# Optimization experiments

Measured on AMD Instinct MI355X. Metric: run time of the kernel, lower is better.

The kernel has to match this reference:

```python
import jax, jax.numpy as jnp
import numpy as np

N = 10000   # nodes
E = 100000  # edges
B = 64      # graphs
HID = 128


def setup_inputs() -> dict:
    key = jax.random.key(0)
    ks = iter(jax.random.split(key, 64))
    def nrm(shape, s=0.1):
        return jax.random.normal(next(ks), shape, dtype=jnp.float32) * s
    inp = {}
    inp["x"] = nrm((N, 1), 1.0)
    inp["node_type"] = jax.random.randint(next(ks), (N,), 0, 2)
    inp["edge_index"] = jax.random.randint(next(ks), (2, E), 0, N)
    inp["edge_attr"] = nrm((E, 1), 1.0)
    inp["batch"] = jnp.sort(jax.random.randint(next(ks), (N,), 0, B))
    inp["vp_w"] = nrm((1, HID)); inp["vp_b"] = nrm((HID,))
    inp["type_emb"] = nrm((2, HID))
    def conv(pre, fin, h, c):
        inp[pre + "_wl"] = nrm((fin, h * c)); inp[pre + "_bl"] = nrm((h * c,))
        inp[pre + "_wr"] = nrm((fin, h * c)); inp[pre + "_br"] = nrm((h * c,))
        inp[pre + "_we"] = nrm((1, h * c));  inp[pre + "_att"] = nrm((h, c))
        inp[pre + "_bias"] = nrm((h * c if pre != "c3" else c,))
    conv("c1", HID, 8, HID)
    conv("c2", HID * 8, 2, HID)
    conv("c3", HID * 2, 1, HID)
    inp["m1_w"] = nrm((HID, HID)); inp["m1_b"] = nrm((HID,))
    inp["ln1_g"] = jnp.ones((HID,), jnp.float32); inp["ln1_b"] = jnp.zeros((HID,), jnp.float32)
    inp["m2_w"] = nrm((HID, HID // 2)); inp["m2_b"] = nrm((HID // 2,))
    inp["ln2_g"] = jnp.ones((HID // 2,), jnp.float32); inp["ln2_b"] = jnp.zeros((HID // 2,), jnp.float32)
    inp["m3_w"] = nrm((HID // 2, 1)); inp["m3_b"] = nrm((1,))
    return inp


def _gatv2(x, src, dst, ea, wl, bl, wr, br, we, att, bias, heads, out_ch, concat):
    """PyG GATv2Conv (eval mode): add self-loops (edge_attr fill='mean' over dst),
    attn = (att * leaky_relu(Wl x_src + Wr x_dst + We e)).sum(-1), segment-softmax
    over destination, scatter-add of alpha * Wl x_src."""
    n = x.shape[0]
    ones = jnp.ones((ea.shape[0], 1), ea.dtype)
    deg = jax.ops.segment_sum(ones, dst, num_segments=n)
    loop_attr = jax.ops.segment_sum(ea, dst, num_segments=n) / jnp.maximum(deg, 1.0)
    ar = jnp.arange(n, dtype=src.dtype)
    src2 = jnp.concatenate([src, ar])
    dst2 = jnp.concatenate([dst, ar])
    ea2 = jnp.concatenate([ea, loop_attr], axis=0)
    xl = (x @ wl + bl).reshape(n, heads, out_ch)   # source transform
    xr = (x @ wr + br).reshape(n, heads, out_ch)   # target transform
    e = (ea2 @ we).reshape(-1, heads, out_ch)      # [E2, H, C]
    msg = xl[src2]                                 # [E2, H, C]
    z = jax.nn.leaky_relu(msg + xr[dst2] + e, 0.2)
    score = jnp.einsum('ehc,hc->eh', z, att)       # [E2, H]
    smax = jax.ops.segment_max(score, dst2, num_segments=n)
    ex = jnp.exp(score - smax[dst2])
    denom = jax.ops.segment_sum(ex, dst2, num_segments=n)
    alpha = ex / denom[dst2]
    out = jax.ops.segment_sum(alpha[:, :, None] * msg, dst2, num_segments=n)
    out = out.reshape(n, heads * out_ch) if concat else out.mean(axis=1)
    return out + bias


def _layernorm(v, g, b):
    mu = v.mean(-1, keepdims=True)
    var = v.var(-1, keepdims=True)
    return (v - mu) / jnp.sqrt(var + 1e-5) * g + b


def reference(x, node_type, edge_index, edge_attr, batch,
              vp_w, vp_b, type_emb,
              c1_wl, c1_bl, c1_wr, c1_br, c1_we, c1_att, c1_bias,
              c2_wl, c2_bl, c2_wr, c2_br, c2_we, c2_att, c2_bias,
              c3_wl, c3_bl, c3_wr, c3_br, c3_we, c3_att, c3_bias,
              m1_w, m1_b, ln1_g, ln1_b, m2_w, m2_b, ln2_g, ln2_b, m3_w, m3_b):
    src, dst = edge_index[0], edge_index[1]
    h = x @ vp_w + vp_b + type_emb[node_type]
    h = jax.nn.leaky_relu(_gatv2(h, src, dst, edge_attr, c1_wl, c1_bl, c1_wr, c1_br, c1_we, c1_att, c1_bias, 8, HID, True), 0.2)
    h = jax.nn.leaky_relu(_gatv2(h, src, dst, edge_attr, c2_wl, c2_bl, c2_wr, c2_br, c2_we, c2_att, c2_bias, 2, HID, True), 0.2)
    h = jax.nn.leaky_relu(_gatv2(h, src, dst, edge_attr, c3_wl, c3_bl, c3_wr, c3_br, c3_we, c3_att, c3_bias, 1, HID, False), 0.2)
    # masked global mean pool over node_type == 0
    w = (node_type == 0).astype(h.dtype)
    sums = jax.ops.segment_sum(h * w[:, None], batch, num_segments=B)
    cnts = jax.ops.segment_sum(w, batch, num_segments=B)
    pooled = sums / jnp.maximum(cnts, 1.0)[:, None]
    h1 = jax.nn.leaky_relu(_layernorm(pooled @ m1_w + m1_b, ln1_g, ln1_b), 0.2)
    h2 = jax.nn.leaky_relu(_layernorm(h1 @ m2_w + m2_b, ln2_g, ln2_b), 0.2)
    return (h2 @ m3_w + m3_b).squeeze(-1)
```

## Files before the change

### kernel.cpp

```cpp
#include <hip/hip_runtime.h>
#include <math.h>

#define NN 10000
#define NE 100000
#define E2 (NE + NN)
#define NBATCH 64

typedef short bf16x8 __attribute__((ext_vector_type(8)));
typedef float f32x4 __attribute__((ext_vector_type(4)));

__device__ __forceinline__ float lrelu(float v){ return v > 0.f ? v : 0.2f*v; }

__device__ __forceinline__ unsigned short f2bf(float x){
  unsigned int u = __float_as_uint(x);
  u += 0x7fffu + ((u >> 16) & 1u);
  return (unsigned short)(u >> 16);
}
__device__ __forceinline__ float bf2f(unsigned short u){
  return __uint_as_float(((unsigned int)u) << 16);
}

__global__ __launch_bounds__(256) void prep_kernel(
    const float* __restrict__ vp_w, const float* __restrict__ vp_b,
    const float* __restrict__ type_emb,
    const float* __restrict__ c1_wl, const float* __restrict__ c1_bl,
    const float* __restrict__ c1_wr, const float* __restrict__ c1_br,
    float* __restrict__ Ul, float* __restrict__ CTl,
    float* __restrict__ Ur, float* __restrict__ CT2,
    const float* __restrict__ c2_wl, const float* __restrict__ c2_wr,
    const float* __restrict__ c3_wl, const float* __restrict__ c3_wr,
    unsigned short* __restrict__ W2lT, unsigned short* __restrict__ W2rT,
    unsigned short* __restrict__ W3lT, unsigned short* __restrict__ W3rT,
    float* __restrict__ zbase, int zero_words)
{
  __shared__ float t[64][65];
  int b = blockIdx.x;
  int tid = threadIdx.x;
  if (b < 144){
    const float* in; unsigned short* out; int K, N, idx;
    if (b < 64)      { in=c2_wl; out=W2lT; K=1024; N=256; idx=b; }
    else if (b <128) { in=c2_wr; out=W2rT; K=1024; N=256; idx=b-64; }
    else if (b <136) { in=c3_wl; out=W3lT; K=256;  N=128; idx=b-128; }
    else             { in=c3_wr; out=W3rT; K=256;  N=128; idx=b-136; }
    int K64 = K >> 6;
    int kx = idx % K64, nx = idx / K64;
    int k0 = kx*64, n0 = nx*64;
    int lr = tid >> 4;
    int lc = (tid & 15) * 4;
#pragma unroll
    for (int i=0;i<4;++i){
      int r = lr + i*16;
      float4 v = *(const float4*)(in + (size_t)(k0+r)*N + n0 + lc);
      t[r][lc+0]=v.x; t[r][lc+1]=v.y; t[r][lc+2]=v.z; t[r][lc+3]=v.w;
    }
    __syncthreads();
    int sr = tid >> 3;
    int sc = (tid & 7) * 8;
#pragma unroll
    for (int i=0;i<2;++i){
      int n = sr + i*32;
      unsigned short tmp[8];
#pragma unroll
      for (int j=0;j<8;++j) tmp[j] = f2bf(t[sc+j][n]);
      unsigned short* op = out + (size_t)(n0+n)*K + k0 + sc;
      *(ushort4*)op       = make_ushort4(tmp[0],tmp[1],tmp[2],tmp[3]);
      *(ushort4*)(op + 4) = make_ushort4(tmp[4],tmp[5],tmp[6],tmp[7]);
    }
  } else if (b < 148){
    int j = (b-144)*256 + tid;
    float ul=0.f, c0l=0.f, c1l=0.f, ur=0.f, c0r=0.f, c1r=0.f;
    for (int k=0; k<128; ++k){
      float a = c1_wl[k*1024 + j], bb = c1_wr[k*1024 + j];
      float vw = vp_w[k], vb = vp_b[k], t0 = type_emb[k], t1 = type_emb[128+k];
      ul += vw*a; ur += vw*bb;
      c0l += (vb+t0)*a; c1l += (vb+t1)*a;
      c0r += (vb+t0)*bb; c1r += (vb+t1)*bb;
    }
    float bl = c1_bl[j], br = c1_br[j];
    Ul[j]=ul; Ur[j]=ur;
    CTl[j]      = c0l + bl;
    CTl[1024+j] = c1l + bl;
    CT2[j]        = (c0l+bl) + (c0r+br);
    CT2[1024+j]   = (c0l+bl) + (c1r+br);
    CT2[2048+j]   = (c1l+bl) + (c0r+br);
    CT2[3072+j]   = (c1l+bl) + (c1r+br);
  } else {
    for (int i = (b-148)*256 + tid; i < zero_words; i += 32*256)
      zbase[i] = 0.f;
  }
}

__global__ void count_kernel(const int* __restrict__ dst, const float* __restrict__ ea,
                             int* __restrict__ deg, float* __restrict__ loop_sum){
  int e = blockIdx.x*256 + threadIdx.x;
  if (e < NE){
    int d = dst[e];
    atomicAdd(&deg[d], 1);
    atomicAdd(&loop_sum[d], ea[e]);
  }
}

__global__ __launch_bounds__(1024) void scan_kernel(const int* __restrict__ deg,
    const float* __restrict__ loop_sum, int* __restrict__ rowptr, float* __restrict__ loop_attr){
  __shared__ int wsum[16];
  __shared__ int carry_s;
  int tid = threadIdx.x;
  int lane = tid & 63, wid = tid >> 6;
  if (tid == 0) carry_s = 0;
  __syncthreads();
  for (int base = 0; base < NN; base += 1024){
    int i = base + tid;
    int v = (i < NN) ? deg[i] : 0;
    int incl = v;
#pragma unroll
    for (int off = 1; off < 64; off <<= 1){
      int t = __shfl_up(incl, off, 64);
      if (lane >= off) incl += t;
    }
    if (lane == 63) wsum[wid] = incl;
    __syncthreads();
    int pre = carry_s;
    for (int w = 0; w < wid; ++w) pre += wsum[w];
    if (i < NN){
      rowptr[i] = pre + incl - v;
      loop_attr[i] = loop_sum[i] / fmaxf((float)v, 1.f);
    }
    __syncthreads();
    if (tid == 0){
      int t = 0;
      for (int w = 0; w < 16; ++w) t += wsum[w];
      carry_s += t;
    }
    __syncthreads();
  }
  if (tid == 0) rowptr[NN] = carry_s;
}

__global__ void fill_kernel(const int* __restrict__ src, const int* __restrict__ dst,
                            const float* __restrict__ ea, const int* __restrict__ rowptr,
                            int* __restrict__ rowctr, int* __restrict__ srcs,
                            int* __restrict__ dsts, float* __restrict__ eav){
  int e = blockIdx.x*256 + threadIdx.x;
  if (e < NE){
    int d = dst[e];
    int p = rowptr[d] + atomicAdd(&rowctr[d], 1);
    srcs[p] = src[e];
    dsts[p] = d;
    eav[p] = ea[e];
  }
}

__global__ __launch_bounds__(256) void conv1_score(
    const int* __restrict__ srcs, const int* __restrict__ dsts, const float* __restrict__ eav,
    const float* __restrict__ loop_attr, const float* __restrict__ x, const int* __restrict__ ntype,
    const float* __restrict__ Ul, const float* __restrict__ Ur, const float* __restrict__ CT2,
    const float* __restrict__ we, const float* __restrict__ att,
    float* __restrict__ scores)
{
  __shared__ float ldsct[4096];
  int tid = threadIdx.x;
  for (int i = tid; i < 1024; i += 256)
    *(float4*)&ldsct[i*4] = *(const float4*)&CT2[i*4];
  int te = tid & 127;
  int sub = tid >> 7;
  int ch0 = te * 8;
  float ul[8], ur[8], wev[8], atv[8];
#pragma unroll
  for (int v=0; v<8; ++v){
    ul[v]=Ul[ch0+v]; ur[v]=Ur[ch0+v]; wev[v]=we[ch0+v]; atv[v]=att[ch0+v];
  }
  __syncthreads();
  for (int j = blockIdx.x*2 + sub; j < E2; j += gridDim.x*2){
    int s, d; float ea;
    if (j < NE){ s = srcs[j]; d = dsts[j]; ea = eav[j]; }
    else       { s = j - NE;  d = s;       ea = loop_attr[s]; }
    float xs = x[s], xn = x[d];
    int tt = ntype[s]*2 + ntype[d];
    const float* cp = &ldsct[tt*1024 + ch0];
    float4 c0 = *(const float4*)cp;
    float4 c1 = *(const float4*)(cp+4);
    float ct[8] = {c0.x,c0.y,c0.z,c0.w,c1.x,c1.y,c1.z,c1.w};
    float p = 0.f;
#pragma unroll
    for (int v=0; v<8; ++v){
      float z = fmaf(xs, ul[v], fmaf(xn, ur[v], fmaf(ea, wev[v], ct[v])));
      p += atv[v]*lrelu(z);
    }
#pragma unroll
    for (int mm=1; mm<16; mm<<=1) p += __shfl_xor(p, mm, 16);
    if ((te & 15) == 0) scores[(size_t)j*8 + (te>>4)] = p;
  }
}

__global__ __launch_bounds__(256) void conv1_agg(
    const int* __restrict__ rowptr, const int* __restrict__ srcs,
    const float* __restrict__ scores, const float* __restrict__ x, const int* __restrict__ ntype,
    const float* __restrict__ Ul, const float* __restrict__ CTl,
    const float* __restrict__ bias, unsigned short* __restrict__ out)
{
  int n = blockIdx.x;
  int tid = threadIdx.x;
  int h = tid >> 5, el = tid & 31;
  int beg = rowptr[n], deg = rowptr[n+1] - beg;
  int cnt = deg + 1;
  float m = -1e30f, l = 0.f, s1 = 0.f, s20 = 0.f;
  for (int i = el; i < cnt; i += 32){
    int pos; int s;
    if (i < deg){ pos = beg + i; s = srcs[pos]; }
    else        { pos = NE + n;  s = n; }
    float p = scores[(size_t)pos*8 + h];
    float xs = x[s];
    float w0 = (ntype[s] == 0) ? 1.f : 0.f;
    float mn = fmaxf(m, p), f = __expf(m-mn), pe = __expf(p-mn);
    l = l*f + pe; s1 = s1*f + pe*xs; s20 = s20*f + pe*w0; m = mn;
  }
#pragma unroll
  for (int off=1; off<32; off<<=1){
    float mb = __shfl_xor(m, off, 32), lb = __shfl_xor(l, off, 32);
    float s1b = __shfl_xor(s1, off, 32), s20b = __shfl_xor(s20, off, 32);
    float mn = fmaxf(m, mb), fa = __expf(m-mn), fb = __expf(mb-mn);
    l = l*fa + lb*fb; s1 = s1*fa + s1b*fb; s20 = s20*fa + s20b*fb; m = mn;
  }
  float inv = 1.f/l;
  s1 *= inv; s20 *= inv;
  float s21 = 1.f - s20;
  int ch0 = tid * 4;
  float4 u  = *(const float4*)(Ul + ch0);
  float4 t0 = *(const float4*)(CTl + ch0);
  float4 t1 = *(const float4*)(CTl + 1024 + ch0);
  float4 bi = *(const float4*)(bias + ch0);
  ushort4 o;
  o.x = f2bf(lrelu(s1*u.x + s20*t0.x + s21*t1.x + bi.x));
  o.y = f2bf(lrelu(s1*u.y + s20*t0.y + s21*t1.y + bi.y));
  o.z = f2bf(lrelu(s1*u.z + s20*t0.z + s21*t1.z + bi.z));
  o.w = f2bf(lrelu(s1*u.w + s20*t0.w + s21*t1.w + bi.w));
  *(ushort4*)(out + (size_t)n*1024 + ch0) = o;
}

template<int H, int THREADS, int VPT, bool ONLY0, bool OUTBF, bool INBF>
__global__ __launch_bounds__(THREADS) void conv_kernel(
    const int* __restrict__ rowptr, const int* __restrict__ srcs, const float* __restrict__ eav,
    const float* __restrict__ loop_attr, const int* __restrict__ ntype,
    const void* __restrict__ Xv, int stride, int xr_off,
    const float* __restrict__ we, const float* __restrict__ att, const float* __restrict__ bias,
    void* __restrict__ out)
{
  const int HC = THREADS*VPT;
  const int TPH = THREADS/H;
  int n = blockIdx.x;
  if (ONLY0 && ntype[n] != 0) return;
  int tid = threadIdx.x;
  int ch0 = tid * VPT;
  const float* Xf = (const float*)Xv;
  const unsigned short* Xb = (const unsigned short*)Xv;
  float wev[VPT], atv[VPT], biv[VPT], xrv[VPT];
#pragma unroll
  for (int v=0; v<VPT; ++v){
    int ch = ch0+v;
    wev[v]=we[ch]; atv[v]=att[ch]; biv[v]=bias[ch];
  }
  if constexpr (INBF){
    ushort4 q = *(const ushort4*)(Xb + (size_t)n*stride + xr_off + ch0);
    xrv[0]=bf2f(q.x); xrv[1]=bf2f(q.y); xrv[2]=bf2f(q.z); xrv[3]=bf2f(q.w);
  } else {
#pragma unroll
    for (int v=0; v<VPT; ++v) xrv[v]=Xf[(size_t)n*stride + xr_off + ch0+v];
  }
  float ms[4], ls[4], A[4][VPT];
#pragma unroll
  for (int k=0; k<4; ++k){
    ms[k] = -INFINITY; ls[k] = 0.f;
#pragma unroll
    for (int v=0; v<VPT; ++v) A[k][v] = 0.f;
  }
  int beg=rowptr[n], end=rowptr[n+1];
  float la = loop_attr[n];
  for (int j=beg; j<=end; j+=4){
    bool val[4]; int sx[4]; float ex[4];
#pragma unroll
    for (int k=0; k<4; ++k){
      int pos = j + k;
      val[k] = pos <= end;
      sx[k] = (!val[k] || pos == end) ? n : srcs[pos];
      ex[k] = !val[k] ? 0.f : (pos == end ? la : eav[pos]);
    }
    float xv[4][VPT];
#pragma unroll
    for (int k=0; k<4; ++k){
      if constexpr (INBF){
        ushort4 q = *(const ushort4*)(Xb + (size_t)sx[k]*stride + ch0);
        xv[k][0]=bf2f(q.x); xv[k][1]=bf2f(q.y); xv[k][2]=bf2f(q.z); xv[k][3]=bf2f(q.w);
      } else if constexpr (VPT == 4){
        float4 q = *(const float4*)(Xf + (size_t)sx[k]*stride + ch0);
        xv[k][0]=q.x; xv[k][1]=q.y; xv[k][2]=q.z; xv[k][3]=q.w;
      } else {
        float2 q = *(const float2*)(Xf + (size_t)sx[k]*stride + ch0);
        xv[k][0]=q.x; xv[k][1]=q.y;
      }
    }
    float p[4];
#pragma unroll
    for (int k=0; k<4; ++k){
      float acc = 0.f;
#pragma unroll
      for (int v=0; v<VPT; ++v)
        acc += atv[v]*lrelu(xv[k][v]+xrv[v]+ex[k]*wev[v]);
      p[k] = acc;
    }
#pragma unroll
    for (int mm=1; mm<TPH; mm<<=1){
#pragma unroll
      for (int k=0; k<4; ++k) p[k] += __shfl_xor(p[k], mm, 64);
    }
#pragma unroll
    for (int k=0; k<4; ++k){
      if (val[k]){
        float mn=fmaxf(ms[k],p[k]), sc=__expf(ms[k]-mn), pe=__expf(p[k]-mn);
        ls[k]=ls[k]*sc+pe; ms[k]=mn;
#pragma unroll
        for (int v=0; v<VPT; ++v) A[k][v]=A[k][v]*sc+pe*xv[k][v];
      }
    }
  }
#pragma unroll
  for (int k=1; k<4; ++k){
    float mn = fmaxf(ms[0], ms[k]);
    float fa = __expf(ms[0]-mn), fb = __expf(ms[k]-mn);
    ls[0] = ls[0]*fa + ls[k]*fb;
#pragma unroll
    for (int v=0; v<VPT; ++v) A[0][v] = A[0][v]*fa + A[k][v]*fb;
    ms[0] = mn;
  }
  float inv = 1.f/ls[0];
  size_t baseo=(size_t)n*HC+ch0;
  if constexpr (OUTBF){
    unsigned short* ob = (unsigned short*)out;
    ushort4 o;
    o.x = f2bf(lrelu(A[0][0]*inv+biv[0]));
    o.y = f2bf(lrelu(A[0][1]*inv+biv[1]));
    o.z = f2bf(lrelu(A[0][2]*inv+biv[2]));
    o.w = f2bf(lrelu(A[0][3]*inv+biv[3]));
    *(ushort4*)(ob + baseo) = o;
  } else {
    float* of = (float*)out;
#pragma unroll
    for (int v=0; v<VPT; ++v) of[baseo+v]=lrelu(A[0][v]*inv+biv[v]);
  }
}

template<bool OUTBF>
__global__ __launch_bounds__(256) void gemm_dual_lds(
    const short* __restrict__ Abf,
    const short* __restrict__ WlT, const short* __restrict__ WrT,
    const float* __restrict__ bl, const float* __restrict__ br,
    void* __restrict__ Out, int M, int K, int NcH, int cgrid, int rgrid)
{
  __shared__ short lds[12288];
  int id = blockIdx.x;
  int xcd = id & 7, slot = id >> 3;
  int nb = slot % cgrid;
  int rowgroup = (slot / cgrid) * 8 + xcd;
  if (rowgroup >= rgrid) return;
  int row0 = rowgroup * 128;
  int NC2 = 2*NcH;
  int halfx = NcH >> 6;
  int isR = nb >= halfx;
  const short* WT = isR ? WrT : WlT;
  const float* bias = isR ? br : bl;
  int col0 = (nb - (isR ? halfx : 0)) * 64;
  int gcol0 = nb * 64;
  int tid = threadIdx.x;
  int lane = tid & 63, wave = tid >> 6;
  int wm = wave >> 1, wn = wave & 1;
  int quad = lane >> 4, l16 = lane & 15;

  const short* asrc[4];
#pragma unroll
  for (int i=0;i<4;++i){
    int c = wave*256 + i*64 + lane;
    int m = c >> 3, j = c & 7;
    int gr = row0 + m; gr = gr < M ? gr : M-1;
    asrc[i] = Abf + (size_t)gr*K + ((j ^ (m & 7)) << 3);
  }
  const short* bsrc[2];
#pragma unroll
  for (int i=0;i<2;++i){
    int c = wave*128 + i*64 + lane;
    int nloc = c >> 3, j = c & 7;
    bsrc[i] = WT + (size_t)(col0 + nloc)*K + ((j ^ (nloc & 7)) << 3);
  }

  float biasv[2] = { bias[col0 + wn*32 + l16], bias[col0 + wn*32 + 16 + l16] };
  f32x4 acc[4][2];
#pragma unroll
  for (int f=0; f<4; ++f)
#pragma unroll
    for (int g=0; g<2; ++g) acc[f][g] = (f32x4){0.f,0.f,0.f,0.f};

  int niter = K >> 6;
  for (int it=0; it<niter; ++it){
    int k0 = it << 6;
#pragma unroll
    for (int i=0;i<4;++i)
      __builtin_amdgcn_global_load_lds(asrc[i] + k0, &lds[(wave*256 + i*64)*8], 16, 0, 0);
#pragma unroll
    for (int i=0;i<2;++i)
      __builtin_amdgcn_global_load_lds(bsrc[i] + k0, &lds[8192 + (wave*128 + i*64)*8], 16, 0, 0);
    __syncthreads();
#pragma unroll
    for (int s=0; s<2; ++s){
      int t = s*4 + quad;
      bf16x8 af[4], bfv[2];
#pragma unroll
      for (int f=0; f<4; ++f){
        int m = wm*64 + f*16 + l16;
        af[f] = *(const bf16x8*)&lds[m*64 + ((t ^ (m & 7)) << 3)];
      }
#pragma unroll
      for (int g=0; g<2; ++g){
        int nloc = wn*32 + g*16 + l16;
        bfv[g] = *(const bf16x8*)&lds[8192 + nloc*64 + ((t ^ (nloc & 7)) << 3)];
      }
#pragma unroll
      for (int f=0; f<4; ++f)
#pragma unroll
        for (int g=0; g<2; ++g)
          acc[f][g] = __builtin_amdgcn_mfma_f32_16x16x32_bf16(af[f], bfv[g], acc[f][g], 0,0,0);
    }
    __syncthreads();
  }

#pragma unroll
  for (int f=0; f<4; ++f){
    int rbase = row0 + wm*64 + f*16 + quad*4;
#pragma unroll
    for (int r=0; r<4; ++r){
      int rr = rbase + r;
      if (rr < M){
#pragma unroll
        for (int g=0; g<2; ++g){
          int cc = gcol0 + wn*32 + g*16 + l16;
          float val = acc[f][g][r] + biasv[g];
          if constexpr (OUTBF) ((unsigned short*)Out)[(size_t)rr*NC2 + cc] = f2bf(val);
          else                 ((float*)Out)[(size_t)rr*NC2 + cc] = val;
        }
      }
    }
  }
}

__device__ __forceinline__ int lbound(const int* __restrict__ a, int n, int key){
  int lo = 0, hi = n;
  while (lo < hi){ int mid = (lo+hi) >> 1; if (a[mid] < key) lo = mid+1; else hi = mid; }
  return lo;
}

__global__ __launch_bounds__(128) void head_kernel(
    const float* __restrict__ h3, const int* __restrict__ ntype, const int* __restrict__ batch,
    const float* __restrict__ m1w, const float* __restrict__ m1b,
    const float* __restrict__ g1, const float* __restrict__ b1,
    const float* __restrict__ m2w, const float* __restrict__ m2b,
    const float* __restrict__ g2, const float* __restrict__ b2,
    const float* __restrict__ m3w, const float* __restrict__ m3b,
    float* __restrict__ out)
{
  __shared__ float p[128];
  __shared__ float hb[128];
  __shared__ float red[128];
  int b = blockIdx.x, j = threadIdx.x;
  int lo = lbound(batch, NN, b);
  int hi = lbound(batch, NN, b+1);
  float s = 0.f, cnt = 0.f;
  int n = lo;
  for (; n + 3 < hi; n += 4){
    float w0 = (ntype[n]   == 0) ? 1.f : 0.f;
    float w1 = (ntype[n+1] == 0) ? 1.f : 0.f;
    float w2 = (ntype[n+2] == 0) ? 1.f : 0.f;
    float w3 = (ntype[n+3] == 0) ? 1.f : 0.f;
    s += w0*h3[(size_t)n*128 + j]     + w1*h3[(size_t)(n+1)*128 + j]
       + w2*h3[(size_t)(n+2)*128 + j] + w3*h3[(size_t)(n+3)*128 + j];
    cnt += w0 + w1 + w2 + w3;
  }
  for (; n < hi; ++n){
    float w = (ntype[n] == 0) ? 1.f : 0.f;
    s += w*h3[(size_t)n*128 + j];
    cnt += w;
  }
  p[j] = s / fmaxf(cnt, 1.f);
  __syncthreads();
  float a = m1b[j];
  for (int k=0; k<128; ++k) a += p[k]*m1w[k*128 + j];
  red[j] = a; __syncthreads();
  for (int off=64; off>0; off>>=1){ if (j<off) red[j] += red[j+off]; __syncthreads(); }
  float mu = red[0] * (1.f/128.f);
  __syncthreads();
  float d = a - mu;
  red[j] = d*d; __syncthreads();
  for (int off=64; off>0; off>>=1){ if (j<off) red[j] += red[j+off]; __syncthreads(); }
  float var = red[0] * (1.f/128.f);
  __syncthreads();
  hb[j] = lrelu(d * rsqrtf(var + 1e-5f) * g1[j] + b1[j]);
  __syncthreads();
  float a2 = 0.f;
  if (j < 64){
    a2 = m2b[j];
    for (int k=0; k<128; ++k) a2 += hb[k]*m2w[k*64 + j];
  }
  red[j] = (j<64) ? a2 : 0.f; __syncthreads();
  for (int off=64; off>0; off>>=1){ if (j<off) red[j] += red[j+off]; __syncthreads(); }
  float mu2 = red[0] * (1.f/64.f);
  __syncthreads();
  float d2 = a2 - mu2;
  red[j] = (j<64) ? d2*d2 : 0.f; __syncthreads();
  for (int off=64; off>0; off>>=1){ if (j<off) red[j] += red[j+off]; __syncthreads(); }
  float var2 = red[0] * (1.f/64.f);
  __syncthreads();
  if (j < 64) hb[j] = lrelu(d2 * rsqrtf(var2 + 1e-5f) * g2[j] + b2[j]);
  __syncthreads();
  if (j == 0){
    float o = m3b[0];
    for (int k=0; k<64; ++k) o += hb[k]*m3w[k];
    out[b] = o;
  }
}

extern "C" void kernel_launch(void* const* d_in, const int* in_sizes, int n_in,
                              void* d_out, int out_size, void* d_ws, size_t ws_size,
                              hipStream_t stream)
{
  const float* x        = (const float*)d_in[0];
  const int*   ntype    = (const int*)d_in[1];
  const int*   ei       = (const int*)d_in[2];
  const float* eattr    = (const float*)d_in[3];
  const int*   batch    = (const int*)d_in[4];
  const float* vp_w     = (const float*)d_in[5];
  const float* vp_b     = (const float*)d_in[6];
  const float* type_emb = (const float*)d_in[7];
  const float* c1_wl = (const float*)d_in[8];  const float* c1_bl = (const float*)d_in[9];
  const float* c1_wr = (const float*)d_in[10]; const float* c1_br = (const float*)d_in[11];
  const float* c1_we = (const float*)d_in[12]; const float* c1_att= (const float*)d_in[13];
  const float* c1_bias=(const float*)d_in[14];
  const float* c2_wl = (const float*)d_in[15]; const float* c2_bl = (const float*)d_in[16];
  const float* c2_wr = (const float*)d_in[17]; const float* c2_br = (const float*)d_in[18];
  const float* c2_we = (const float*)d_in[19]; const float* c2_att= (const float*)d_in[20];
  const float* c2_bias=(const float*)d_in[21];
  const float* c3_wl = (const float*)d_in[22]; const float* c3_bl = (const float*)d_in[23];
  const float* c3_wr = (const float*)d_in[24]; const float* c3_br = (const float*)d_in[25];
  const float* c3_we = (const float*)d_in[26]; const float* c3_att= (const float*)d_in[27];
  const float* c3_bias=(const float*)d_in[28];
  const float* m1_w = (const float*)d_in[29]; const float* m1_b = (const float*)d_in[30];
  const float* ln1_g= (const float*)d_in[31]; const float* ln1_b= (const float*)d_in[32];
  const float* m2_w = (const float*)d_in[33]; const float* m2_b = (const float*)d_in[34];
  const float* ln2_g= (const float*)d_in[35]; const float* ln2_b= (const float*)d_in[36];
  const float* m3_w = (const float*)d_in[37]; const float* m3_b = (const float*)d_in[38];
  const int* esrc = ei;
  const int* edst = ei + NE;
  float* outp = (float*)d_out;
  (void)in_sizes; (void)n_in; (void)out_size; (void)ws_size;

  char* w = (char*)d_ws;
  auto alloc = [&](size_t bytes) -> void* {
    void* p = (void*)w;
    w += (bytes + 255) & ~(size_t)255;
    return p;
  };
  unsigned short* h1bf = (unsigned short*)alloc((size_t)NN*1024*2);
  unsigned short* X2   = (unsigned short*)alloc((size_t)NN*512*2);
  unsigned short* h2bf = (unsigned short*)alloc((size_t)NN*256*2);
  float* X3   = (float*)alloc((size_t)NN*256*4);
  float* h3   = (float*)alloc((size_t)NN*128*4);
  unsigned short* W2lT = (unsigned short*)alloc((size_t)256*1024*2);
  unsigned short* W2rT = (unsigned short*)alloc((size_t)256*1024*2);
  unsigned short* W3lT = (unsigned short*)alloc((size_t)128*256*2);
  unsigned short* W3rT = (unsigned short*)alloc((size_t)128*256*2);
  float* Ul   = (float*)alloc(1024*4);
  float* CTl  = (float*)alloc(2048*4);
  float* Ur   = (float*)alloc(1024*4);
  float* CT2  = (float*)alloc(4096*4);
  float* scores = (float*)alloc((size_t)E2*8*4);
  const int zero_words = 3*NN;
  float* zbase = (float*)alloc((size_t)zero_words*4);
  int*   deg      = (int*)zbase;
  int*   rowctr   = (int*)(zbase + NN);
  float* loop_sum = zbase + 2*NN;
  float* loop_attr= (float*)alloc((size_t)NN*4);
  int*   rowptr   = (int*)alloc((size_t)(NN+1)*4);
  int*   srcs     = (int*)alloc((size_t)NE*4);
  int*   dsts     = (int*)alloc((size_t)NE*4);
  float* eav      = (float*)alloc((size_t)NE*4);

  prep_kernel<<<180, 256, 0, stream>>>(vp_w, vp_b, type_emb,
      c1_wl, c1_bl, c1_wr, c1_br, Ul, CTl, Ur, CT2,
      c2_wl, c2_wr, c3_wl, c3_wr, W2lT, W2rT, W3lT, W3rT,
      zbase, zero_words);
  count_kernel<<<(NE+255)/256, 256, 0, stream>>>(edst, eattr, deg, loop_sum);
  scan_kernel<<<1, 1024, 0, stream>>>(deg, loop_sum, rowptr, loop_attr);
  fill_kernel<<<(NE+255)/256, 256, 0, stream>>>(esrc, edst, eattr, rowptr, rowctr,
                                                srcs, dsts, eav);
  conv1_score<<<2048, 256, 0, stream>>>(srcs, dsts, eav, loop_attr, x, ntype,
      Ul, Ur, CT2, c1_we, c1_att, scores);
  conv1_agg<<<NN, 256, 0, stream>>>(rowptr, srcs, scores, x, ntype,
      Ul, CTl, c1_bias, h1bf);
  gemm_dual_lds<true><<<640, 256, 0, stream>>>(
      (const short*)h1bf, (const short*)W2lT, (const short*)W2rT, c2_bl, c2_br,
      (void*)X2, NN, 1024, 256, 8, 79);
  conv_kernel<2,64,4,false,true,true><<<NN, 64, 0, stream>>>(rowptr, srcs, eav, loop_attr, ntype,
      (const void*)X2, 512, 256, c2_we, c2_att, c2_bias, h2bf);
  gemm_dual_lds<false><<<320, 256, 0, stream>>>(
      (const short*)h2bf, (const short*)W3lT, (const short*)W3rT, c3_bl, c3_br,
      (void*)X3, NN, 256, 128, 4, 79);
  conv_kernel<1,64,2,true,false,false><<<NN, 64, 0, stream>>>(rowptr, srcs, eav, loop_attr, ntype,
      (const void*)X3, 256, 128, c3_we, c3_att, c3_bias, h3);
  head_kernel<<<NBATCH, 128, 0, stream>>>(h3, ntype, batch, m1_w, m1_b, ln1_g, ln1_b,
                                          m2_w, m2_b, ln2_g, ln2_b, m3_w, m3_b, outp);
}
```

Before: 321.2 us.

## Split conv2/conv3 into edge-parallel score and node-parallel aggregate kernels

Replaces the single per-node online-softmax conv kernel for layers 2 and 3 with two passes. An edge-parallel kernel computes attention logits into a scores buffer, then a per-node kernel stages scores and sources in LDS, does a two-pass softmax, and aggregates with 4-way unrolled gathers. This is meant to remove the serial per-edge online-softmax rescaling and the latency of one block walking a long edge list, at the cost of a scores round trip through memory and an extra launch per layer. Nodes with in-degree above 1023 are silently truncated by the 1024-entry LDS cap.

```diff
diff --git a/kernel.cpp b/kernel.cpp
--- a/kernel.cpp
+++ b/kernel.cpp
@@ -237,115 +237,177 @@
   *(ushort4*)(out + (size_t)n*1024 + ch0) = o;
 }
 
-template<int H, int THREADS, int VPT, bool ONLY0, bool OUTBF, bool INBF>
-__global__ __launch_bounds__(THREADS) void conv_kernel(
-    const int* __restrict__ rowptr, const int* __restrict__ srcs, const float* __restrict__ eav,
+__global__ __launch_bounds__(256) void conv2_score(
+    const int* __restrict__ srcs, const int* __restrict__ dsts, const float* __restrict__ eav,
+    const float* __restrict__ loop_attr, const unsigned short* __restrict__ X2,
+    const float* __restrict__ we, const float* __restrict__ att,
+    float* __restrict__ scores2)
+{
+  int tid = threadIdx.x;
+  int lane = tid & 63, wv = tid >> 6;
+  int half = lane >> 5;
+  int ch0 = (lane & 31)*4 + half*128;
+  float wev[4], atv[4];
+#pragma unroll
+  for (int v=0; v<4; ++v){ wev[v]=we[ch0+v]; atv[v]=att[ch0+v]; }
+  for (int j = blockIdx.x*4 + wv; j < E2; j += gridDim.x*4){
+    int s, d; float ea;
+    if (j < NE){ s = srcs[j]; d = dsts[j]; ea = eav[j]; }
+    else       { s = j - NE;  d = s;       ea = loop_attr[s]; }
+    ushort4 ql = *(const ushort4*)(X2 + (size_t)s*512 + ch0);
+    ushort4 qr = *(const ushort4*)(X2 + (size_t)d*512 + 256 + ch0);
+    float xl[4] = {bf2f(ql.x),bf2f(ql.y),bf2f(ql.z),bf2f(ql.w)};
+    float xr[4] = {bf2f(qr.x),bf2f(qr.y),bf2f(qr.z),bf2f(qr.w)};
+    float p = 0.f;
+#pragma unroll
+    for (int v=0; v<4; ++v) p += atv[v]*lrelu(xl[v]+xr[v]+ea*wev[v]);
+#pragma unroll
+    for (int mm=1; mm<32; mm<<=1) p += __shfl_xor(p, mm, 64);
+    if ((lane & 31) == 0) scores2[(size_t)j*2 + half] = p;
+  }
+}
+
+__global__ __launch_bounds__(64) void conv2_agg(
+    const int* __restrict__ rowptr, const int* __restrict__ srcs,
+    const float* __restrict__ scores2, const unsigned short* __restrict__ X2,
+    const float* __restrict__ bias, unsigned short* __restrict__ out)
+{
+  __shared__ float pe2[1024][2];
+  __shared__ int es[1024];
+  int n = blockIdx.x, tid = threadIdx.x;
+  int beg = rowptr[n], deg = rowptr[n+1] - beg;
+  int cnt = deg + 1; if (cnt > 1024) cnt = 1024;
+  float m0 = -1e30f, m1 = -1e30f;
+  for (int i = tid; i < cnt; i += 64){
+    int pos = (i < deg) ? beg + i : NE + n;
+    float2 sc = *(const float2*)(scores2 + (size_t)pos*2);
+    pe2[i][0] = sc.x; pe2[i][1] = sc.y;
+    es[i] = (i < deg) ? srcs[pos] : n;
+    m0 = fmaxf(m0, sc.x); m1 = fmaxf(m1, sc.y);
+  }
+#pragma unroll
+  for (int off=1; off<64; off<<=1){
+    m0 = fmaxf(m0, __shfl_xor(m0, off, 64));
+    m1 = fmaxf(m1, __shfl_xor(m1, off, 64));
+  }
+  __syncthreads();
+  float l0 = 0.f, l1 = 0.f;
+  for (int i = tid; i < cnt; i += 64){
+    float e0 = __expf(pe2[i][0]-m0), e1 = __expf(pe2[i][1]-m1);
+    pe2[i][0] = e0; pe2[i][1] = e1;
+    l0 += e0; l1 += e1;
+  }
+#pragma unroll
+  for (int off=1; off<64; off<<=1){
+    l0 += __shfl_xor(l0, off, 64);
+    l1 += __shfl_xor(l1, off, 64);
+  }
+  __syncthreads();
+  int ch0 = tid*4, h = tid >> 5;
+  float inv = 1.f/((h==0) ? l0 : l1);
+  float acc[4] = {0.f,0.f,0.f,0.f};
+  int e = 0;
+  for (; e + 3 < cnt; e += 4){
+    float a0=pe2[e][h], a1=pe2[e+1][h], a2=pe2[e+2][h], a3=pe2[e+3][h];
+    int s0=es[e], s1=es[e+1], s2=es[e+2], s3=es[e+3];
+    ushort4 q0 = *(const ushort4*)(X2 + (size_t)s0*512 + ch0);
+    ushort4 q1 = *(const ushort4*)(X2 + (size_t)s1*512 + ch0);
+    ushort4 q2 = *(const ushort4*)(X2 + (size_t)s2*512 + ch0);
+    ushort4 q3 = *(const ushort4*)(X2 + (size_t)s3*512 + ch0);
+    acc[0] += a0*bf2f(q0.x) + a1*bf2f(q1.x) + a2*bf2f(q2.x) + a3*bf2f(q3.x);
+    acc[1] += a0*bf2f(q0.y) + a1*bf2f(q1.y) + a2*bf2f(q2.y) + a3*bf2f(q3.y);
+    acc[2] += a0*bf2f(q0.z) + a1*bf2f(q1.z) + a2*bf2f(q2.z) + a3*bf2f(q3.z);
+    acc[3] += a0*bf2f(q0.w) + a1*bf2f(q1.w) + a2*bf2f(q2.w) + a3*bf2f(q3.w);
+  }
+  for (; e < cnt; ++e){
+    float a = pe2[e][h];
+    ushort4 q = *(const ushort4*)(X2 + (size_t)es[e]*512 + ch0);
+    acc[0]+=a*bf2f(q.x); acc[1]+=a*bf2f(q.y); acc[2]+=a*bf2f(q.z); acc[3]+=a*bf2f(q.w);
+  }
+  ushort4 o;
+  o.x = f2bf(lrelu(acc[0]*inv + bias[ch0+0]));
+  o.y = f2bf(lrelu(acc[1]*inv + bias[ch0+1]));
+  o.z = f2bf(lrelu(acc[2]*inv + bias[ch0+2]));
+  o.w = f2bf(lrelu(acc[3]*inv + bias[ch0+3]));
+  *(ushort4*)(out + (size_t)n*256 + ch0) = o;
+}
+
+__global__ __launch_bounds__(256) void conv3_score(
+    const int* __restrict__ srcs, const int* __restrict__ dsts, const float* __restrict__ eav,
     const float* __restrict__ loop_attr, const int* __restrict__ ntype,
-    const void* __restrict__ Xv, int stride, int xr_off,
-    const float* __restrict__ we, const float* __restrict__ att, const float* __restrict__ bias,
-    void* __restrict__ out)
-{
-  const int HC = THREADS*VPT;
-  const int TPH = THREADS/H;
-  int n = blockIdx.x;
-  if (ONLY0 && ntype[n] != 0) return;
+    const float* __restrict__ X3,
+    const float* __restrict__ we, const float* __restrict__ att,
+    float* __restrict__ scores3)
+{
   int tid = threadIdx.x;
-  int ch0 = tid * VPT;
-  const float* Xf = (const float*)Xv;
-  const unsigned short* Xb = (const unsigned short*)Xv;
-  float wev[VPT], atv[VPT], biv[VPT], xrv[VPT];
-#pragma unroll
-  for (int v=0; v<VPT; ++v){
-    int ch = ch0+v;
-    wev[v]=we[ch]; atv[v]=att[ch]; biv[v]=bias[ch];
-  }
-  if constexpr (INBF){
-    ushort4 q = *(const ushort4*)(Xb + (size_t)n*stride + xr_off + ch0);
-    xrv[0]=bf2f(q.x); xrv[1]=bf2f(q.y); xrv[2]=bf2f(q.z); xrv[3]=bf2f(q.w);
-  } else {
-#pragma unroll
-    for (int v=0; v<VPT; ++v) xrv[v]=Xf[(size_t)n*stride + xr_off + ch0+v];
-  }
-  float ms[4], ls[4], A[4][VPT];
-#pragma unroll
-  for (int k=0; k<4; ++k){
-    ms[k] = -INFINITY; ls[k] = 0.f;
-#pragma unroll
-    for (int v=0; v<VPT; ++v) A[k][v] = 0.f;
-  }
-  int beg=rowptr[n], end=rowptr[n+1];
-  float la = loop_attr[n];
-  for (int j=beg; j<=end; j+=4){
-    bool val[4]; int sx[4]; float ex[4];
-#pragma unroll
-    for (int k=0; k<4; ++k){
-      int pos = j + k;
-      val[k] = pos <= end;
-      sx[k] = (!val[k] || pos == end) ? n : srcs[pos];
-      ex[k] = !val[k] ? 0.f : (pos == end ? la : eav[pos]);
-    }
-    float xv[4][VPT];
-#pragma unroll
-    for (int k=0; k<4; ++k){
-      if constexpr (INBF){
-        ushort4 q = *(const ushort4*)(Xb + (size_t)sx[k]*stride + ch0);
-        xv[k][0]=bf2f(q.x); xv[k][1]=bf2f(q.y); xv[k][2]=bf2f(q.z); xv[k][3]=bf2f(q.w);
-      } else if constexpr (VPT == 4){
-        float4 q = *(const float4*)(Xf + (size_t)sx[k]*stride + ch0);
-        xv[k][0]=q.x; xv[k][1]=q.y; xv[k][2]=q.z; xv[k][3]=q.w;
-      } else {
-        float2 q = *(const float2*)(Xf + (size_t)sx[k]*stride + ch0);
-        xv[k][0]=q.x; xv[k][1]=q.y;
-      }
-    }
-    float p[4];
-#pragma unroll
-    for (int k=0; k<4; ++k){
-      float acc = 0.f;
-#pragma unroll
-      for (int v=0; v<VPT; ++v)
-        acc += atv[v]*lrelu(xv[k][v]+xrv[v]+ex[k]*wev[v]);
-      p[k] = acc;
-    }
-#pragma unroll
-    for (int mm=1; mm<TPH; mm<<=1){
-#pragma unroll
-      for (int k=0; k<4; ++k) p[k] += __shfl_xor(p[k], mm, 64);
-    }
-#pragma unroll
-    for (int k=0; k<4; ++k){
-      if (val[k]){
-        float mn=fmaxf(ms[k],p[k]), sc=__expf(ms[k]-mn), pe=__expf(p[k]-mn);
-        ls[k]=ls[k]*sc+pe; ms[k]=mn;
-#pragma unroll
-        for (int v=0; v<VPT; ++v) A[k][v]=A[k][v]*sc+pe*xv[k][v];
-      }
-    }
-  }
-#pragma unroll
-  for (int k=1; k<4; ++k){
-    float mn = fmaxf(ms[0], ms[k]);
-    float fa = __expf(ms[0]-mn), fb = __expf(ms[k]-mn);
-    ls[0] = ls[0]*fa + ls[k]*fb;
-#pragma unroll
-    for (int v=0; v<VPT; ++v) A[0][v] = A[0][v]*fa + A[k][v]*fb;
-    ms[0] = mn;
-  }
-  float inv = 1.f/ls[0];
-  size_t baseo=(size_t)n*HC+ch0;
-  if constexpr (OUTBF){
-    unsigned short* ob = (unsigned short*)out;
-    ushort4 o;
-    o.x = f2bf(lrelu(A[0][0]*inv+biv[0]));
-    o.y = f2bf(lrelu(A[0][1]*inv+biv[1]));
-    o.z = f2bf(lrelu(A[0][2]*inv+biv[2]));
-    o.w = f2bf(lrelu(A[0][3]*inv+biv[3]));
-    *(ushort4*)(ob + baseo) = o;
-  } else {
-    float* of = (float*)out;
-#pragma unroll
-    for (int v=0; v<VPT; ++v) of[baseo+v]=lrelu(A[0][v]*inv+biv[v]);
-  }
+  int lane = tid & 63, wv = tid >> 6;
+  int ch0 = lane*2;
+  float wev[2] = {we[ch0], we[ch0+1]};
+  float atv[2] = {att[ch0], att[ch0+1]};
+  for (int j = blockIdx.x*4 + wv; j < E2; j += gridDim.x*4){
+    int s, d; float ea;
+    if (j < NE){ s = srcs[j]; d = dsts[j]; ea = eav[j]; }
+    else       { s = j - NE;  d = s;       ea = loop_attr[s]; }
+    if (ntype[d] != 0) continue;
+    float2 ql = *(const float2*)(X3 + (size_t)s*256 + ch0);
+    float2 qr = *(const float2*)(X3 + (size_t)d*256 + 128 + ch0);
+    float p = atv[0]*lrelu(ql.x+qr.x+ea*wev[0]) + atv[1]*lrelu(ql.y+qr.y+ea*wev[1]);
+#pragma unroll
+    for (int mm=1; mm<64; mm<<=1) p += __shfl_xor(p, mm, 64);
+    if (lane == 0) scores3[j] = p;
+  }
+}
+
+__global__ __launch_bounds__(64) void conv3_agg(
+    const int* __restrict__ rowptr, const int* __restrict__ srcs, const int* __restrict__ ntype,
+    const float* __restrict__ scores3, const float* __restrict__ X3,
+    const float* __restrict__ bias, float* __restrict__ out)
+{
+  __shared__ float pe[1024];
+  __shared__ int es[1024];
+  int n = blockIdx.x, tid = threadIdx.x;
+  if (ntype[n] != 0) return;
+  int beg = rowptr[n], deg = rowptr[n+1] - beg;
+  int cnt = deg + 1; if (cnt > 1024) cnt = 1024;
+  float m = -1e30f;
+  for (int i = tid; i < cnt; i += 64){
+    int pos = (i < deg) ? beg + i : NE + n;
+    float sc = scores3[pos];
+    pe[i] = sc;
+    es[i] = (i < deg) ? srcs[pos] : n;
+    m = fmaxf(m, sc);
+  }
+#pragma unroll
+  for (int off=1; off<64; off<<=1) m = fmaxf(m, __shfl_xor(m, off, 64));
+  __syncthreads();
+  float l = 0.f;
+  for (int i = tid; i < cnt; i += 64){
+    float e0 = __expf(pe[i]-m);
+    pe[i] = e0; l += e0;
+  }
+#pragma unroll
+  for (int off=1; off<64; off<<=1) l += __shfl_xor(l, off, 64);
+  __syncthreads();
+  int ch0 = tid*2;
+  float inv = 1.f/l;
+  float acc0 = 0.f, acc1 = 0.f;
+  int e = 0;
+  for (; e + 3 < cnt; e += 4){
+    float a0=pe[e], a1=pe[e+1], a2=pe[e+2], a3=pe[e+3];
+    float2 q0 = *(const float2*)(X3 + (size_t)es[e]*256 + ch0);
+    float2 q1 = *(const float2*)(X3 + (size_t)es[e+1]*256 + ch0);
+    float2 q2 = *(const float2*)(X3 + (size_t)es[e+2]*256 + ch0);
+    float2 q3 = *(const float2*)(X3 + (size_t)es[e+3]*256 + ch0);
+    acc0 += a0*q0.x + a1*q1.x + a2*q2.x + a3*q3.x;
+    acc1 += a0*q0.y + a1*q1.y + a2*q2.y + a3*q3.y;
+  }
+  for (; e < cnt; ++e){
+    float a = pe[e];
+    float2 q = *(const float2*)(X3 + (size_t)es[e]*256 + ch0);
+    acc0 += a*q.x; acc1 += a*q.y;
+  }
+  out[(size_t)n*128 + ch0]     = lrelu(acc0*inv + bias[ch0]);
+  out[(size_t)n*128 + ch0 + 1] = lrelu(acc1*inv + bias[ch0+1]);
 }
 
 template<bool OUTBF>
@@ -577,7 +639,9 @@
   float* CTl  = (float*)alloc(2048*4);
   float* Ur   = (float*)alloc(1024*4);
   float* CT2  = (float*)alloc(4096*4);
-  float* scores = (float*)alloc((size_t)E2*8*4);
+  float* scores  = (float*)alloc((size_t)E2*8*4);
+  float* scores2 = (float*)alloc((size_t)E2*2*4);
+  float* scores3 = (float*)alloc((size_t)E2*4);
   const int zero_words = 3*NN;
   float* zbase = (float*)alloc((size_t)zero_words*4);
   int*   deg      = (int*)zbase;
@@ -604,13 +668,15 @@
   gemm_dual_lds<true><<<640, 256, 0, stream>>>(
       (const short*)h1bf, (const short*)W2lT, (const short*)W2rT, c2_bl, c2_br,
       (void*)X2, NN, 1024, 256, 8, 79);
-  conv_kernel<2,64,4,false,true,true><<<NN, 64, 0, stream>>>(rowptr, srcs, eav, loop_attr, ntype,
-      (const void*)X2, 512, 256, c2_we, c2_att, c2_bias, h2bf);
+  conv2_score<<<2048, 256, 0, stream>>>(srcs, dsts, eav, loop_attr, X2,
+      c2_we, c2_att, scores2);
+  conv2_agg<<<NN, 64, 0, stream>>>(rowptr, srcs, scores2, X2, c2_bias, h2bf);
   gemm_dual_lds<false><<<320, 256, 0, stream>>>(
       (const short*)h2bf, (const short*)W3lT, (const short*)W3rT, c3_bl, c3_br,
       (void*)X3, NN, 256, 128, 4, 79);
-  conv_kernel<1,64,2,true,false,false><<<NN, 64, 0, stream>>>(rowptr, srcs, eav, loop_attr, ntype,
-      (const void*)X3, 256, 128, c3_we, c3_att, c3_bias, h3);
+  conv3_score<<<1024, 256, 0, stream>>>(srcs, dsts, eav, loop_attr, ntype, X3,
+      c3_we, c3_att, scores3);
+  conv3_agg<<<NN, 64, 0, stream>>>(rowptr, srcs, ntype, scores3, X3, c3_bias, h3);
   head_kernel<<<NBATCH, 128, 0, stream>>>(h3, ntype, batch, m1_w, m1_b, ln1_g, ln1_b,
                                           m2_w, m2_b, ln2_g, ln2_b, m3_w, m3_b, outp);
 }
```

After: 350.6 us. +9.1%, slower.
